# Performance work log

Measured on AMD Instinct MI355X. Metric: run time of the kernel, lower is better.

The kernel has to match this reference:

```python
import jax, jax.numpy as jnp
import numpy as np

N = 8192      # atoms
E = 131072    # edges (avg degree 16)
C = 32        # channels per irrep
Z = 10        # num_elements
G = 16        # num_graphs
NB = 8        # num_bessel
NSH = 9       # spherical harmonic components for max_ell=2 (1+3+5)
R_MAX = 5.0
P_CUT = 5     # num_polynomial_cutoff
AVG_NEIGH = 16.0
LMAP = np.array([0, 1, 1, 1, 2, 2, 2, 2, 2])  # m-component -> l index


def _sph(u):
    # real spherical harmonics up to l=2, 'component' normalization, unit input
    x, y, z = u[:, 0], u[:, 1], u[:, 2]
    s3, s5, s15 = 3.0 ** 0.5, 5.0 ** 0.5, 15.0 ** 0.5
    return jnp.stack([
        jnp.ones_like(x),
        s3 * x, s3 * y, s3 * z,
        s15 * x * y, s15 * y * z, (s5 / 2) * (3 * z * z - 1.0),
        s15 * x * z, (s15 / 2) * (x * x - y * y),
    ], axis=1)  # [E, 9]


def _radial(r):
    # Bessel radial basis with smooth polynomial cutoff (MACE RadialEmbeddingBlock)
    n = jnp.arange(1, NB + 1, dtype=r.dtype)  # [NB]
    pref = (2.0 / R_MAX) ** 0.5
    bessel = pref * jnp.sin(n[None, :] * jnp.pi * r[:, None] / R_MAX) / r[:, None]
    x = r / R_MAX
    p = float(P_CUT)
    env = (1.0 - (p + 1.0) * (p + 2.0) / 2.0 * x ** P_CUT
           + p * (p + 2.0) * x ** (P_CUT + 1)
           - p * (p + 1.0) / 2.0 * x ** (P_CUT + 2))
    env = env * (x < 1.0)
    return bessel * env[:, None]  # [E, NB]


def setup_inputs() -> dict:
    key = jax.random.key(0)
    k = jax.random.split(key, 24)
    positions = jax.random.normal(k[0], (N, 3), dtype=jnp.float32) * 2.0
    species = jax.random.randint(k[1], (N,), 0, Z)
    node_attrs = jax.nn.one_hot(species, Z, dtype=jnp.float32)
    edge_index = jax.random.randint(k[2], (2, E), 0, N, dtype=jnp.int32)
    batch = jnp.sort(jax.random.randint(k[3], (N,), 0, G, dtype=jnp.int32))
    charges = jax.random.normal(k[4], (N,), dtype=jnp.float32) * 0.1
    sd = 0.1
    atomic_energies = jax.random.normal(k[5], (Z,), dtype=jnp.float32)
    W_embed = jax.random.normal(k[6], (Z, C), dtype=jnp.float32) * sd
    R0 = jax.random.normal(k[7], (2, NB, 64), dtype=jnp.float32) / np.sqrt(NB)
    R1 = jax.random.normal(k[8], (2, 64, 64), dtype=jnp.float32) / 8.0
    R2 = jax.random.normal(k[9], (2, 64, 64), dtype=jnp.float32) / 8.0
    R3 = jax.random.normal(k[10], (2, 64, 3 * C), dtype=jnp.float32) / 8.0
    W_mix = jax.random.normal(k[11], (2, 3, C, C), dtype=jnp.float32) / np.sqrt(C)
    W_sc = jax.random.normal(k[12], (2, 3, C, C), dtype=jnp.float32) / np.sqrt(C)
    Wp1 = jax.random.normal(k[13], (2, Z, C), dtype=jnp.float32) * 0.5
    Wp2 = jax.random.normal(k[14], (2, Z, C), dtype=jnp.float32) * 0.5
    Wp3 = jax.random.normal(k[15], (2, Z, C), dtype=jnp.float32) * 0.5
    wE1 = jax.random.normal(k[16], (C,), dtype=jnp.float32) * sd
    wD1 = jax.random.normal(k[17], (C,), dtype=jnp.float32) * sd
    Wh = jax.random.normal(k[18], (C, 16), dtype=jnp.float32) / np.sqrt(C)
    wE2 = jax.random.normal(k[19], (16,), dtype=jnp.float32) * sd
    wD2 = jax.random.normal(k[20], (C,), dtype=jnp.float32) * sd
    return dict(positions=positions, node_attrs=node_attrs, charges=charges,
                atomic_energies=atomic_energies, W_embed=W_embed,
                R0=R0, R1=R1, R2=R2, R3=R3, W_mix=W_mix, W_sc=W_sc,
                Wp1=Wp1, Wp2=Wp2, Wp3=Wp3, wE1=wE1, wD1=wD1, Wh=Wh,
                wE2=wE2, wD2=wD2, edge_index=edge_index, batch=batch)


def reference(positions, node_attrs, charges, atomic_energies, W_embed,
              R0, R1, R2, R3, W_mix, W_sc, Wp1, Wp2, Wp3,
              wE1, wD1, Wh, wE2, wD2, edge_index, batch):
    snd, rcv = edge_index[0], edge_index[1]
    lmap = jnp.asarray(LMAP)

    # edge geometry
    vec = positions[rcv] - positions[snd]          # [E,3]
    r = jnp.sqrt(jnp.sum(vec * vec, axis=1) + 1e-12)
    Y = _sph(vec / r[:, None])                     # [E,9]
    rb = _radial(r)                                # [E,NB]

    # atomic reference energies e0
    node_e0 = node_attrs @ atomic_energies         # [N]
    e_tot = jax.ops.segment_sum(node_e0, batch, num_segments=G)

    # node embedding (scalar channels), lifted into full irrep layout [N,9,C]
    h0 = node_attrs @ W_embed
    h = jnp.zeros((N, NSH, C), h0.dtype).at[:, 0, :].set(h0)

    dip = jnp.zeros((N, 3), positions.dtype)
    for i in range(2):
        # radial MLP -> per-edge, per-l tensor-product weights
        x = jax.nn.silu(rb @ R0[i])
        x = jax.nn.silu(x @ R1[i])
        x = jax.nn.silu(x @ R2[i])
        Rw = (x @ R3[i]).reshape(E, 3, C)[:, lmap, :]       # [E,9,C]
        # edge-wise tensor product: scalar node feats x SH, radially weighted
        hs = h[:, 0, :]                                      # [N,C]
        msg = Rw * Y[:, :, None] * hs[snd][:, None, :]       # [E,9,C]
        # scatter-sum message passing
        A = jax.ops.segment_sum(msg, rcv, num_segments=N) / AVG_NEIGH
        A = jnp.einsum('nmc,mcd->nmd', A, W_mix[i][lmap])    # per-l linear
        sc = jnp.einsum('nmc,mcd->nmd', h, W_sc[i][lmap])    # self-connection
        # symmetric product basis (correlation 3, element-dependent weights)
        s = A[:, 0, :]
        w1 = node_attrs @ Wp1[i]
        w2 = node_attrs @ Wp2[i]
        w3 = node_attrs @ Wp3[i]
        B = A * (w1[:, None, :] + w2[:, None, :] * s[:, None, :]
                 + w3[:, None, :] * (s * s)[:, None, :])
        h = B + sc
        # readouts: energy from 0e channels, dipole from 1o channels
        if i == 0:
            e_node = h[:, 0, :] @ wE1
            d_node = jnp.einsum('nmc,c->nm', h[:, 1:4, :], wD1)
        else:
            hid = jax.nn.silu(h[:, 0, :] @ Wh)
            e_node = hid @ wE2
            d_node = jnp.einsum('nmc,c->nm', h[:, 1:4, :], wD2)
        e_tot = e_tot + jax.ops.segment_sum(e_node, batch, num_segments=G)
        dip = dip + d_node

    total_dipole = jax.ops.segment_sum(dip, batch, num_segments=G)
    total_dipole = total_dipole + jax.ops.segment_sum(
        charges[:, None] * positions, batch, num_segments=G)  # fixed-charge baseline
    return jnp.concatenate([e_tot[:, None], total_dipole], axis=1)  # [G,4]
```

## Files before the change

kernel.cpp:

```cpp
#include <hip/hip_runtime.h>
#include <math.h>

#define N_NODES 8192
#define N_EDGES 131072
#define C 32
#define Zn 10
#define NG 16
#define NB 8
#define H 64
#define TABN 4096
#define PPB 32
#define XS 73
#define NPB 8
#define CAP 64
#define SL 48

__device__ __forceinline__ float silu_f(float v){ return v / (1.0f + __expf(-v)); }

__global__ __launch_bounds__(256)
void prep_kernel(const float* __restrict__ pos, const int* __restrict__ ei,
                 int* __restrict__ cursor, int* __restrict__ bucket,
                 const float* __restrict__ na, const float* __restrict__ Wemb,
                 int* __restrict__ species, float* __restrict__ hg,
                 const float* __restrict__ R0g, const float* __restrict__ R1g,
                 const float* __restrict__ R2g, const float* __restrict__ R3g,
                 float2* __restrict__ Tab2, float* __restrict__ out){
  __shared__ float xsh[PPB*XS];
  __shared__ int spec_lds[64];
  int b = blockIdx.x;
  int tid = threadIdx.x;

  if (b >= 258){
    if (b < 386){
      int n0 = (b-258)*64;
      if (tid < 64){
        int n = n0 + tid;
        int spec = 0;
        #pragma unroll
        for (int z = 1; z < Zn; z++) if (na[n*Zn+z] > 0.5f) spec = z;
        species[n] = spec;
        spec_lds[tid] = spec;
      }
      if (b == 258 && tid >= 64 && tid < 128) out[tid-64] = 0.f;
      __syncthreads();
      float4* dst = (float4*)(hg + (size_t)n0*288);
      const float4 z4 = make_float4(0.f,0.f,0.f,0.f);
      #pragma unroll
      for (int it = 0; it < 18; it++){
        int f = it*256 + tid;
        int node = f / 72;
        int q = f - node*72;
        float4 v = z4;
        if (q < 8) v = ((const float4*)(Wemb + spec_lds[node]*C))[q];
        dst[f] = v;
      }
    } else {
      int e = (b-386)*256 + tid;
      int snd = ei[e], rcv = ei[N_EDGES + e];
      float px = pos[rcv*3+0]-pos[snd*3+0];
      float py = pos[rcv*3+1]-pos[snd*3+1];
      float pz = pos[rcv*3+2]-pos[snd*3+2];
      float r2 = px*px+py*py+pz*pz;
      if (r2 < 25.0f){
        int slot = atomicAdd(cursor + rcv, 1);
        if (slot < CAP) bucket[rcv*CAP + slot] = snd;
      }
    }
    return;
  }

  int tb = b;
  const int nb = (TABN + PPB)/PPB;
  int half = tb / nb;
  int blk  = tb - half*nb;
  const float* R0i = R0g + half*NB*H;
  const float* R1i = R1g + half*H*H;
  const float* R2i = R2g + half*H*H;
  const float* R3i = R3g + half*H*96;
  float2* TabH = Tab2 + (size_t)half*((size_t)TABN*96);

  int pl = tid >> 3, jt = tid & 7;
  int i = blk*PPB + pl;
  float r = (i == 0) ? 1e-6f : (float)i * (5.0f/TABN);
  {
    float xr = r*0.2f;
    float env = 0.f;
    if (xr < 1.0f){
      float x2 = xr*xr, x5 = x2*x2*xr;
      env = 1.f - 21.f*x5 + 35.f*x5*xr - 15.f*x5*x2;
    }
    float sc = 0.6324555320336759f / r * env;
    xsh[pl*XS + jt] = sc * sinf((float)(jt+1)*0.6283185307179586f*r);
  }
  __syncthreads();

  float acc[12];
  #pragma unroll
  for (int j = 0; j < 8; j++) acc[j] = 0.f;
  #pragma unroll
  for (int k = 0; k < 8; k++){
    float xk = xsh[pl*XS + k];
    const float4* w4 = (const float4*)(R0i + k*H + jt*8);
    float4 wa = w4[0], wb = w4[1];
    acc[0]=fmaf(xk,wa.x,acc[0]); acc[1]=fmaf(xk,wa.y,acc[1]);
    acc[2]=fmaf(xk,wa.z,acc[2]); acc[3]=fmaf(xk,wa.w,acc[3]);
    acc[4]=fmaf(xk,wb.x,acc[4]); acc[5]=fmaf(xk,wb.y,acc[5]);
    acc[6]=fmaf(xk,wb.z,acc[6]); acc[7]=fmaf(xk,wb.w,acc[7]);
  }
  __syncthreads();
  #pragma unroll
  for (int j = 0; j < 8; j++) xsh[pl*XS + jt*8 + j] = silu_f(acc[j]);
  __syncthreads();

  const float* Wl[2] = {R1i, R2i};
  #pragma unroll
  for (int L = 0; L < 2; L++){
    const float* W = Wl[L];
    #pragma unroll
    for (int j = 0; j < 8; j++) acc[j] = 0.f;
    #pragma unroll 8
    for (int k = 0; k < H; k++){
      float xk = xsh[pl*XS + k];
      const float4* w4 = (const float4*)(W + k*H + jt*8);
      float4 wa = w4[0], wb = w4[1];
      acc[0]=fmaf(xk,wa.x,acc[0]); acc[1]=fmaf(xk,wa.y,acc[1]);
      acc[2]=fmaf(xk,wa.z,acc[2]); acc[3]=fmaf(xk,wa.w,acc[3]);
      acc[4]=fmaf(xk,wb.x,acc[4]); acc[5]=fmaf(xk,wb.y,acc[5]);
      acc[6]=fmaf(xk,wb.z,acc[6]); acc[7]=fmaf(xk,wb.w,acc[7]);
    }
    __syncthreads();
    #pragma unroll
    for (int j = 0; j < 8; j++) xsh[pl*XS + jt*8 + j] = silu_f(acc[j]);
    __syncthreads();
  }

  #pragma unroll
  for (int j = 0; j < 12; j++) acc[j] = 0.f;
  #pragma unroll 8
  for (int k = 0; k < H; k++){
    float xk = xsh[pl*XS + k];
    const float4* w4 = (const float4*)(R3i + k*96 + jt*12);
    float4 wa = w4[0], wb = w4[1], wc = w4[2];
    acc[0]=fmaf(xk,wa.x,acc[0]);  acc[1]=fmaf(xk,wa.y,acc[1]);
    acc[2]=fmaf(xk,wa.z,acc[2]);  acc[3]=fmaf(xk,wa.w,acc[3]);
    acc[4]=fmaf(xk,wb.x,acc[4]);  acc[5]=fmaf(xk,wb.y,acc[5]);
    acc[6]=fmaf(xk,wb.z,acc[6]);  acc[7]=fmaf(xk,wb.w,acc[7]);
    acc[8]=fmaf(xk,wc.x,acc[8]);  acc[9]=fmaf(xk,wc.y,acc[9]);
    acc[10]=fmaf(xk,wc.z,acc[10]); acc[11]=fmaf(xk,wc.w,acc[11]);
  }
  if (i <= TABN){
    int cb = jt*12;
    #pragma unroll
    for (int j = 0; j < 12; j++){
      int c = cb + j;
      float val = acc[j];
      if (i < TABN) TabH[(size_t)i*96 + c].x = val;
      if (i > 0)    TabH[(size_t)(i-1)*96 + c].y = val;
    }
  }
}

__global__ __launch_bounds__(512)
void node_kernel(const float2* __restrict__ Tab2, const int* __restrict__ bucket,
                 const int* __restrict__ deg,
                 const float* __restrict__ hg_in, float* __restrict__ hg_out,
                 const float* __restrict__ Wm_g, const float* __restrict__ Ws_g,
                 const float* __restrict__ Wp1, const float* __restrict__ Wp2,
                 const float* __restrict__ Wp3,
                 const int* __restrict__ species, const int* __restrict__ batch,
                 const float* __restrict__ ae, const float* __restrict__ charges,
                 const float* __restrict__ pos,
                 const float* __restrict__ wEv, const float* __restrict__ wDv,
                 const float* __restrict__ Whg, const float* __restrict__ wE2g,
                 int iter, float* __restrict__ out){
  __shared__ float abuf[NPB][288];
  __shared__ float sbuf[NPB][288];
  __shared__ float glds[NG][4];
  float* estage = &sbuf[0][0];
  int tid = threadIdx.x;
  if (tid < NG*4) glds[tid>>2][tid&3] = 0.f;
  int w = tid >> 6, lane = tid & 63;
  int c31 = lane & 31;
  bool hi = lane >= 32;
  int ng0 = blockIdx.x*NPB;
  int n = ng0 + w;

  int cnt = deg[n]; if (cnt > SL) cnt = SL;
  if (lane < cnt){
    int snd = bucket[n*CAP + lane];
    float px = pos[n*3+0] - pos[snd*3+0];
    float py = pos[n*3+1] - pos[snd*3+1];
    float pz = pos[n*3+2] - pos[snd*3+2];
    float r = sqrtf(px*px+py*py+pz*pz + 1e-12f);
    float inv = 1.0f/r;
    float* es = estage + (w*SL + lane)*6;
    es[0] = px*inv; es[1] = py*inv; es[2] = pz*inv;
    es[3] = r * (TABN/5.0f);
    es[4] = __int_as_float(snd);
  }

  const float s3 = 1.7320508075688772f;
  const float s5 = 2.23606797749979f;
  const float s15 = 3.872983346207417f;
  int colA = (hi ? 32 : 0) + c31;
  int colB = 32 + c31;
  int colC = 64 + c31;
  float acc0=0.f, acc1=0.f, acc2=0.f, acc3=0.f, acc4=0.f;
  #pragma unroll 4
  for (int j = 0; j < cnt; j++){
    const float* es = estage + (w*SL + j)*6;
    float x = es[0], y = es[1], z = es[2], u = es[3];
    int snd = __float_as_int(es[4]);
    int i0 = (int)u;
    if (i0 > TABN-1) i0 = TABN-1;
    float f = u - (float)i0;
    const float2* T2 = Tab2 + (size_t)i0*96;
    float hs = hg_in[(size_t)snd*288 + c31];
    float2 ta = T2[colA];
    float2 tb = T2[colB];
    float2 tc = T2[colC];
    float wv0 = fmaf(ta.y - ta.x, f, ta.x) * hs;
    float wv1 = fmaf(tb.y - tb.x, f, tb.x) * hs;
    float wv2 = fmaf(tc.y - tc.x, f, tc.x) * hs;
    float Ys0 = hi ? s3*x : 1.0f;
    float Ys1 = s3 * (hi ? z : y);
    float Ys2 = s15 * (hi ? y*z : x*y);
    float Ys3 = hi ? s15*x*z : 0.5f*s5*(3.f*z*z - 1.f);
    float Ys4 = 0.5f*s15*(x*x - y*y);
    acc0 = fmaf(wv0, Ys0, acc0);
    acc1 = fmaf(wv1, Ys1, acc1);
    acc2 = fmaf(wv2, Ys2, acc2);
    acc3 = fmaf(wv2, Ys3, acc3);
    acc4 = fmaf(wv2, Ys4, acc4);
  }
  __syncthreads();
  abuf[w][lane]       = acc0 * (1.0f/16.0f);
  abuf[w][lane + 64]  = acc1 * (1.0f/16.0f);
  abuf[w][lane + 128] = acc2 * (1.0f/16.0f);
  abuf[w][lane + 192] = acc3 * (1.0f/16.0f);
  if (!hi) abuf[w][lane + 256] = acc4 * (1.0f/16.0f);
  __syncthreads();

  float a2[NPB], scv[NPB];
  int idx0 = w*64 + lane;
  bool actm = (w < 5) && (idx0 < 288);
  if (w < 5){
    int m = idx0 >> 5; if (m > 8) m = 8;
    int l = (m >= 4) ? 2 : ((m >= 1) ? 1 : 0);
    const float* wmB = Wm_g + l*1024 + c31;
    const float* wsB = Ws_g + l*1024 + c31;
    #pragma unroll
    for (int n2 = 0; n2 < NPB; n2++){ a2[n2] = 0.f; scv[n2] = 0.f; }
    #pragma unroll
    for (int q = 0; q < 8; q++){
      float w0 = wmB[(4*q+0)*32], w1 = wmB[(4*q+1)*32];
      float w2 = wmB[(4*q+2)*32], w3 = wmB[(4*q+3)*32];
      float t0 = wsB[(4*q+0)*32], t1 = wsB[(4*q+1)*32];
      float t2 = wsB[(4*q+2)*32], t3 = wsB[(4*q+3)*32];
      #pragma unroll
      for (int n2 = 0; n2 < NPB; n2++){
        float4 av = *(const float4*)(&abuf[n2][m*32 + 4*q]);
        float4 hv = *(const float4*)(hg_in + (size_t)(ng0+n2)*288 + m*32 + 4*q);
        a2[n2] = fmaf(av.x, w0, a2[n2]); a2[n2] = fmaf(av.y, w1, a2[n2]);
        a2[n2] = fmaf(av.z, w2, a2[n2]); a2[n2] = fmaf(av.w, w3, a2[n2]);
        scv[n2] = fmaf(hv.x, t0, scv[n2]); scv[n2] = fmaf(hv.y, t1, scv[n2]);
        scv[n2] = fmaf(hv.z, t2, scv[n2]); scv[n2] = fmaf(hv.w, t3, scv[n2]);
      }
    }
  }
  __syncthreads();
  if (actm){
    #pragma unroll
    for (int n2 = 0; n2 < NPB; n2++){
      abuf[n2][idx0] = a2[n2];
      sbuf[n2][idx0] = scv[n2];
    }
  }
  __syncthreads();

  int spec = species[n];
  float sval = abuf[w][c31];
  float p1 = Wp1[spec*C+c31], p2 = Wp2[spec*C+c31], p3 = Wp3[spec*C+c31];
  float f = p1 + p2*sval + p3*sval*sval;
  #pragma unroll
  for (int it = 0; it < 5; it++){
    int idx = it*64 + lane;
    if (idx < 288){
      float hn = abuf[w][idx]*f + sbuf[w][idx];
      hg_out[(size_t)n*288 + idx] = hn;
      abuf[w][idx] = hn;
    }
  }

  int g = batch[n];
  float dv0 = 0.f, dv1 = 0.f, dv2 = 0.f, ev = 0.f;
  if (lane < 32){
    dv0 = abuf[w][32+lane]*wDv[lane];
    dv1 = abuf[w][64+lane]*wDv[lane];
    dv2 = abuf[w][96+lane]*wDv[lane];
  }
  if (iter == 0){
    if (lane < 32) ev = abuf[w][lane]*wEv[lane];
  } else {
    if (lane < 16){
      float hid = 0.f;
      #pragma unroll
      for (int c = 0; c < 32; c++) hid = fmaf(abuf[w][c], Whg[c*16+lane], hid);
      hid = silu_f(hid);
      ev = hid * wE2g[lane];
    }
  }
  #pragma unroll
  for (int off = 16; off >= 1; off >>= 1){
    ev  += __shfl_down(ev,  off);
    dv0 += __shfl_down(dv0, off);
    dv1 += __shfl_down(dv1, off);
    dv2 += __shfl_down(dv2, off);
  }
  if (lane == 0){
    if (iter == 0){
      ev += ae[spec];
      float q = charges[n];
      dv0 += q*pos[n*3+0];
      dv1 += q*pos[n*3+1];
      dv2 += q*pos[n*3+2];
    }
    atomicAdd(&glds[g][0], ev);
    atomicAdd(&glds[g][1], dv0);
    atomicAdd(&glds[g][2], dv1);
    atomicAdd(&glds[g][3], dv2);
  }
  __syncthreads();
  if (tid < NG*4){
    float v = glds[tid>>2][tid&3];
    if (v != 0.f) atomicAdd(out + tid, v);
  }
}

extern "C" void kernel_launch(void* const* d_in, const int* in_sizes, int n_in,
                              void* d_out, int out_size, void* d_ws, size_t ws_size,
                              hipStream_t stream){
  const float* positions       = (const float*)d_in[0];
  const float* node_attrs      = (const float*)d_in[1];
  const float* charges         = (const float*)d_in[2];
  const float* atomic_energies = (const float*)d_in[3];
  const float* W_embed         = (const float*)d_in[4];
  const float* R0              = (const float*)d_in[5];
  const float* R1              = (const float*)d_in[6];
  const float* R2              = (const float*)d_in[7];
  const float* R3              = (const float*)d_in[8];
  const float* W_mix           = (const float*)d_in[9];
  const float* W_sc            = (const float*)d_in[10];
  const float* Wp1             = (const float*)d_in[11];
  const float* Wp2             = (const float*)d_in[12];
  const float* Wp3             = (const float*)d_in[13];
  const float* wE1             = (const float*)d_in[14];
  const float* wD1             = (const float*)d_in[15];
  const float* Wh              = (const float*)d_in[16];
  const float* wE2             = (const float*)d_in[17];
  const float* wD2             = (const float*)d_in[18];
  const int*   edge_index      = (const int*)d_in[19];
  const int*   batch           = (const int*)d_in[20];
  float* out = (float*)d_out;

  char* wsp = (char*)d_ws;
  int*    bucket = (int*)wsp;    wsp += sizeof(int)*(size_t)N_NODES*CAP;
  float2* Tab2   = (float2*)wsp; wsp += sizeof(float2)*(size_t)2*TABN*96;
  float*  hg_a   = (float*)wsp;  wsp += sizeof(float)*(size_t)N_NODES*288;
  float*  hg_b   = (float*)wsp;  wsp += sizeof(float)*(size_t)N_NODES*288;
  int* cursor    = (int*)wsp;    wsp += sizeof(int)*N_NODES;
  int* species   = (int*)wsp;    wsp += sizeof(int)*N_NODES;

  hipMemsetAsync(cursor, 0, N_NODES*sizeof(int), stream);

  prep_kernel<<<898, 256, 0, stream>>>(positions, edge_index, cursor, bucket,
                                       node_attrs, W_embed, species, hg_a,
                                       R0, R1, R2, R3, Tab2, out);

  for (int i = 0; i < 2; i++){
    const float* hin  = (i == 0) ? hg_a : hg_b;
    float*       hout = (i == 0) ? hg_b : hg_a;
    node_kernel<<<N_NODES/NPB, 512, 0, stream>>>(Tab2 + (size_t)i*TABN*96, bucket,
                                               cursor, hin, hout,
                                               W_mix + i*3*C*C, W_sc + i*3*C*C,
                                               Wp1 + i*Zn*C, Wp2 + i*Zn*C, Wp3 + i*Zn*C,
                                               species, batch,
                                               atomic_energies, charges, positions,
                                               wE1, (i == 0) ? wD1 : wD2,
                                               Wh, wE2, i, out);
  }
}
```

Before: 206.7 us.

## Store compact initial embedding, skip zero self-connection work and final write

```diff
diff --git a/kernel.cpp b/kernel.cpp
--- a/kernel.cpp
+++ b/kernel.cpp
@@ -9,11 +9,14 @@
 #define NB 8
 #define H 64
 #define TABN 4096
-#define PPB 32
-#define XS 73
+#define TPP 16
 #define NPB 8
 #define CAP 64
 #define SL 48
+
+#define TB_TAB  514
+#define TB_EDGE (TB_TAB + 512)
+#define TB_H0   (TB_EDGE + 128)
 
 __device__ __forceinline__ float silu_f(float v){ return v / (1.0f + __expf(-v)); }
 
@@ -21,41 +24,18 @@
 void prep_kernel(const float* __restrict__ pos, const int* __restrict__ ei,
                  int* __restrict__ cursor, int* __restrict__ bucket,
                  const float* __restrict__ na, const float* __restrict__ Wemb,
-                 int* __restrict__ species, float* __restrict__ hg,
+                 int* __restrict__ species, float* __restrict__ h0c,
                  const float* __restrict__ R0g, const float* __restrict__ R1g,
                  const float* __restrict__ R2g, const float* __restrict__ R3g,
                  float2* __restrict__ Tab2, float* __restrict__ out){
-  __shared__ float xsh[PPB*XS];
+  __shared__ float xsh[TPP*65];
   __shared__ int spec_lds[64];
   int b = blockIdx.x;
   int tid = threadIdx.x;
 
-  if (b >= 258){
-    if (b < 386){
-      int n0 = (b-258)*64;
-      if (tid < 64){
-        int n = n0 + tid;
-        int spec = 0;
-        #pragma unroll
-        for (int z = 1; z < Zn; z++) if (na[n*Zn+z] > 0.5f) spec = z;
-        species[n] = spec;
-        spec_lds[tid] = spec;
-      }
-      if (b == 258 && tid >= 64 && tid < 128) out[tid-64] = 0.f;
-      __syncthreads();
-      float4* dst = (float4*)(hg + (size_t)n0*288);
-      const float4 z4 = make_float4(0.f,0.f,0.f,0.f);
-      #pragma unroll
-      for (int it = 0; it < 18; it++){
-        int f = it*256 + tid;
-        int node = f / 72;
-        int q = f - node*72;
-        float4 v = z4;
-        if (q < 8) v = ((const float4*)(Wemb + spec_lds[node]*C))[q];
-        dst[f] = v;
-      }
-    } else {
-      int e = (b-386)*256 + tid;
+  if (b >= TB_TAB){
+    if (b < TB_EDGE){
+      int e = (b-TB_TAB)*256 + tid;
       int snd = ei[e], rcv = ei[N_EDGES + e];
       float px = pos[rcv*3+0]-pos[snd*3+0];
       float py = pos[rcv*3+1]-pos[snd*3+1];
@@ -65,24 +45,42 @@
         int slot = atomicAdd(cursor + rcv, 1);
         if (slot < CAP) bucket[rcv*CAP + slot] = snd;
       }
+    } else {
+      int n0 = (b-TB_EDGE)*64;
+      if (tid < 64){
+        int n = n0 + tid;
+        int spec = 0;
+        #pragma unroll
+        for (int z = 1; z < Zn; z++) if (na[n*Zn+z] > 0.5f) spec = z;
+        species[n] = spec;
+        spec_lds[tid] = spec;
+      }
+      if (b == TB_EDGE && tid >= 64 && tid < 128) out[tid-64] = 0.f;
+      __syncthreads();
+      float4* dst = (float4*)(h0c + (size_t)n0*32);
+      #pragma unroll
+      for (int it = 0; it < 2; it++){
+        int f = it*256 + tid;
+        int node = f >> 3, q = f & 7;
+        dst[f] = ((const float4*)(Wemb + spec_lds[node]*C))[q];
+      }
     }
     return;
   }
 
-  int tb = b;
-  const int nb = (TABN + PPB)/PPB;
-  int half = tb / nb;
-  int blk  = tb - half*nb;
+  const int nb = 257;
+  int half = (b >= nb) ? 1 : 0;
+  int blk  = b - half*nb;
   const float* R0i = R0g + half*NB*H;
   const float* R1i = R1g + half*H*H;
   const float* R2i = R2g + half*H*H;
   const float* R3i = R3g + half*H*96;
   float2* TabH = Tab2 + (size_t)half*((size_t)TABN*96);
 
-  int pl = tid >> 3, jt = tid & 7;
-  int i = blk*PPB + pl;
+  int pl = tid >> 4, jt = tid & 15;
+  int i = blk*TPP + pl;
   float r = (i == 0) ? 1e-6f : (float)i * (5.0f/TABN);
-  {
+  if (jt < 8){
     float xr = r*0.2f;
     float env = 0.f;
     if (xr < 1.0f){
@@ -90,26 +88,23 @@
       env = 1.f - 21.f*x5 + 35.f*x5*xr - 15.f*x5*x2;
     }
     float sc = 0.6324555320336759f / r * env;
-    xsh[pl*XS + jt] = sc * sinf((float)(jt+1)*0.6283185307179586f*r);
-  }
-  __syncthreads();
-
-  float acc[12];
-  #pragma unroll
-  for (int j = 0; j < 8; j++) acc[j] = 0.f;
+    xsh[pl*65 + jt] = sc * sinf((float)(jt+1)*0.6283185307179586f*r);
+  }
+  __syncthreads();
+
+  float acc[6];
+  #pragma unroll
+  for (int j = 0; j < 4; j++) acc[j] = 0.f;
   #pragma unroll
   for (int k = 0; k < 8; k++){
-    float xk = xsh[pl*XS + k];
-    const float4* w4 = (const float4*)(R0i + k*H + jt*8);
-    float4 wa = w4[0], wb = w4[1];
-    acc[0]=fmaf(xk,wa.x,acc[0]); acc[1]=fmaf(xk,wa.y,acc[1]);
-    acc[2]=fmaf(xk,wa.z,acc[2]); acc[3]=fmaf(xk,wa.w,acc[3]);
-    acc[4]=fmaf(xk,wb.x,acc[4]); acc[5]=fmaf(xk,wb.y,acc[5]);
-    acc[6]=fmaf(xk,wb.z,acc[6]); acc[7]=fmaf(xk,wb.w,acc[7]);
-  }
-  __syncthreads();
-  #pragma unroll
-  for (int j = 0; j < 8; j++) xsh[pl*XS + jt*8 + j] = silu_f(acc[j]);
+    float xk = xsh[pl*65 + k];
+    float4 w = *(const float4*)(R0i + k*H + jt*4);
+    acc[0]=fmaf(xk,w.x,acc[0]); acc[1]=fmaf(xk,w.y,acc[1]);
+    acc[2]=fmaf(xk,w.z,acc[2]); acc[3]=fmaf(xk,w.w,acc[3]);
+  }
+  __syncthreads();
+  #pragma unroll
+  for (int j = 0; j < 4; j++) xsh[pl*65 + jt*4 + j] = silu_f(acc[j]);
   __syncthreads();
 
   const float* Wl[2] = {R1i, R2i};
@@ -117,41 +112,37 @@
   for (int L = 0; L < 2; L++){
     const float* W = Wl[L];
     #pragma unroll
-    for (int j = 0; j < 8; j++) acc[j] = 0.f;
+    for (int j = 0; j < 4; j++) acc[j] = 0.f;
     #pragma unroll 8
     for (int k = 0; k < H; k++){
-      float xk = xsh[pl*XS + k];
-      const float4* w4 = (const float4*)(W + k*H + jt*8);
-      float4 wa = w4[0], wb = w4[1];
-      acc[0]=fmaf(xk,wa.x,acc[0]); acc[1]=fmaf(xk,wa.y,acc[1]);
-      acc[2]=fmaf(xk,wa.z,acc[2]); acc[3]=fmaf(xk,wa.w,acc[3]);
-      acc[4]=fmaf(xk,wb.x,acc[4]); acc[5]=fmaf(xk,wb.y,acc[5]);
-      acc[6]=fmaf(xk,wb.z,acc[6]); acc[7]=fmaf(xk,wb.w,acc[7]);
+      float xk = xsh[pl*65 + k];
+      float4 w = *(const float4*)(W + k*H + jt*4);
+      acc[0]=fmaf(xk,w.x,acc[0]); acc[1]=fmaf(xk,w.y,acc[1]);
+      acc[2]=fmaf(xk,w.z,acc[2]); acc[3]=fmaf(xk,w.w,acc[3]);
     }
     __syncthreads();
     #pragma unroll
-    for (int j = 0; j < 8; j++) xsh[pl*XS + jt*8 + j] = silu_f(acc[j]);
+    for (int j = 0; j < 4; j++) xsh[pl*65 + jt*4 + j] = silu_f(acc[j]);
     __syncthreads();
   }
 
   #pragma unroll
-  for (int j = 0; j < 12; j++) acc[j] = 0.f;
+  for (int j = 0; j < 6; j++) acc[j] = 0.f;
   #pragma unroll 8
   for (int k = 0; k < H; k++){
-    float xk = xsh[pl*XS + k];
-    const float4* w4 = (const float4*)(R3i + k*96 + jt*12);
-    float4 wa = w4[0], wb = w4[1], wc = w4[2];
-    acc[0]=fmaf(xk,wa.x,acc[0]);  acc[1]=fmaf(xk,wa.y,acc[1]);
-    acc[2]=fmaf(xk,wa.z,acc[2]);  acc[3]=fmaf(xk,wa.w,acc[3]);
-    acc[4]=fmaf(xk,wb.x,acc[4]);  acc[5]=fmaf(xk,wb.y,acc[5]);
-    acc[6]=fmaf(xk,wb.z,acc[6]);  acc[7]=fmaf(xk,wb.w,acc[7]);
-    acc[8]=fmaf(xk,wc.x,acc[8]);  acc[9]=fmaf(xk,wc.y,acc[9]);
-    acc[10]=fmaf(xk,wc.z,acc[10]); acc[11]=fmaf(xk,wc.w,acc[11]);
+    float xk = xsh[pl*65 + k];
+    const float* wp = R3i + k*96 + jt*6;
+    float2 w0 = *(const float2*)(wp);
+    float2 w1 = *(const float2*)(wp+2);
+    float2 w2 = *(const float2*)(wp+4);
+    acc[0]=fmaf(xk,w0.x,acc[0]); acc[1]=fmaf(xk,w0.y,acc[1]);
+    acc[2]=fmaf(xk,w1.x,acc[2]); acc[3]=fmaf(xk,w1.y,acc[3]);
+    acc[4]=fmaf(xk,w2.x,acc[4]); acc[5]=fmaf(xk,w2.y,acc[5]);
   }
   if (i <= TABN){
-    int cb = jt*12;
-    #pragma unroll
-    for (int j = 0; j < 12; j++){
+    int cb = jt*6;
+    #pragma unroll
+    for (int j = 0; j < 6; j++){
       int c = cb + j;
       float val = acc[j];
       if (i < TABN) TabH[(size_t)i*96 + c].x = val;
@@ -162,7 +153,7 @@
 
 __global__ __launch_bounds__(512)
 void node_kernel(const float2* __restrict__ Tab2, const int* __restrict__ bucket,
-                 const int* __restrict__ deg,
+                 const int* __restrict__ deg, const float* __restrict__ h0c,
                  const float* __restrict__ hg_in, float* __restrict__ hg_out,
                  const float* __restrict__ Wm_g, const float* __restrict__ Ws_g,
                  const float* __restrict__ Wp1, const float* __restrict__ Wp2,
@@ -215,7 +206,8 @@
     if (i0 > TABN-1) i0 = TABN-1;
     float f = u - (float)i0;
     const float2* T2 = Tab2 + (size_t)i0*96;
-    float hs = hg_in[(size_t)snd*288 + c31];
+    float hs = (iter == 0) ? h0c[(size_t)snd*32 + c31]
+                           : hg_in[(size_t)snd*288 + c31];
     float2 ta = T2[colA];
     float2 tb = T2[colB];
     float2 tc = T2[colC];
@@ -247,6 +239,7 @@
   if (w < 5){
     int m = idx0 >> 5; if (m > 8) m = 8;
     int l = (m >= 4) ? 2 : ((m >= 1) ? 1 : 0);
+    bool needsc = (iter != 0) || (m == 0);
     const float* wmB = Wm_g + l*1024 + c31;
     const float* wsB = Ws_g + l*1024 + c31;
     #pragma unroll
@@ -255,16 +248,23 @@
     for (int q = 0; q < 8; q++){
       float w0 = wmB[(4*q+0)*32], w1 = wmB[(4*q+1)*32];
       float w2 = wmB[(4*q+2)*32], w3 = wmB[(4*q+3)*32];
-      float t0 = wsB[(4*q+0)*32], t1 = wsB[(4*q+1)*32];
-      float t2 = wsB[(4*q+2)*32], t3 = wsB[(4*q+3)*32];
+      float t0 = 0.f, t1 = 0.f, t2 = 0.f, t3 = 0.f;
+      if (needsc){
+        t0 = wsB[(4*q+0)*32]; t1 = wsB[(4*q+1)*32];
+        t2 = wsB[(4*q+2)*32]; t3 = wsB[(4*q+3)*32];
+      }
       #pragma unroll
       for (int n2 = 0; n2 < NPB; n2++){
         float4 av = *(const float4*)(&abuf[n2][m*32 + 4*q]);
-        float4 hv = *(const float4*)(hg_in + (size_t)(ng0+n2)*288 + m*32 + 4*q);
         a2[n2] = fmaf(av.x, w0, a2[n2]); a2[n2] = fmaf(av.y, w1, a2[n2]);
         a2[n2] = fmaf(av.z, w2, a2[n2]); a2[n2] = fmaf(av.w, w3, a2[n2]);
-        scv[n2] = fmaf(hv.x, t0, scv[n2]); scv[n2] = fmaf(hv.y, t1, scv[n2]);
-        scv[n2] = fmaf(hv.z, t2, scv[n2]); scv[n2] = fmaf(hv.w, t3, scv[n2]);
+        if (needsc){
+          float4 hv = (iter == 0)
+            ? *(const float4*)(h0c + (size_t)(ng0+n2)*32 + 4*q)
+            : *(const float4*)(hg_in + (size_t)(ng0+n2)*288 + m*32 + 4*q);
+          scv[n2] = fmaf(hv.x, t0, scv[n2]); scv[n2] = fmaf(hv.y, t1, scv[n2]);
+          scv[n2] = fmaf(hv.z, t2, scv[n2]); scv[n2] = fmaf(hv.w, t3, scv[n2]);
+        }
       }
     }
   }
@@ -287,7 +287,7 @@
     int idx = it*64 + lane;
     if (idx < 288){
       float hn = abuf[w][idx]*f + sbuf[w][idx];
-      hg_out[(size_t)n*288 + idx] = hn;
+      if (iter == 0) hg_out[(size_t)n*288 + idx] = hn;
       abuf[w][idx] = hn;
     }
   }
@@ -366,22 +366,21 @@
   char* wsp = (char*)d_ws;
   int*    bucket = (int*)wsp;    wsp += sizeof(int)*(size_t)N_NODES*CAP;
   float2* Tab2   = (float2*)wsp; wsp += sizeof(float2)*(size_t)2*TABN*96;
-  float*  hg_a   = (float*)wsp;  wsp += sizeof(float)*(size_t)N_NODES*288;
-  float*  hg_b   = (float*)wsp;  wsp += sizeof(float)*(size_t)N_NODES*288;
+  float*  h0c    = (float*)wsp;  wsp += sizeof(float)*(size_t)N_NODES*32;
+  float*  hg_mid = (float*)wsp;  wsp += sizeof(float)*(size_t)N_NODES*288;
   int* cursor    = (int*)wsp;    wsp += sizeof(int)*N_NODES;
   int* species   = (int*)wsp;    wsp += sizeof(int)*N_NODES;
 
   hipMemsetAsync(cursor, 0, N_NODES*sizeof(int), stream);
 
-  prep_kernel<<<898, 256, 0, stream>>>(positions, edge_index, cursor, bucket,
-                                       node_attrs, W_embed, species, hg_a,
-                                       R0, R1, R2, R3, Tab2, out);
+  prep_kernel<<<TB_H0, 256, 0, stream>>>(positions, edge_index, cursor, bucket,
+                                         node_attrs, W_embed, species, h0c,
+                                         R0, R1, R2, R3, Tab2, out);
 
   for (int i = 0; i < 2; i++){
-    const float* hin  = (i == 0) ? hg_a : hg_b;
-    float*       hout = (i == 0) ? hg_b : hg_a;
     node_kernel<<<N_NODES/NPB, 512, 0, stream>>>(Tab2 + (size_t)i*TABN*96, bucket,
-                                               cursor, hin, hout,
+                                               cursor, h0c,
+                                               hg_mid, hg_mid,
                                                W_mix + i*3*C*C, W_sc + i*3*C*C,
                                                Wp1 + i*Zn*C, Wp2 + i*Zn*C, Wp3 + i*Zn*C,
                                                species, batch,
```

After: 322.8 us. 56.2% more time.
